# Optimization experiments

Hardware: AMD Instinct MI355X
Metric: run time of the kernel (lower is better)

## Reference

```python
import jax, jax.numpy as jnp
import numpy as np
from jax import lax

# init_kwargs constants
DO_TUBE = False
TAU = 0.3
ITERATIONS = 5
BLEND_FACTOR = 0.3


def _avg_pool3(x):
    """3x3x3 avg pool, stride 1, zero padding 1, count_include_pad=True.
    x: (n, h, w, d). Matches torch F.avg_pool3d(kernel=3, stride=1, padding=1)."""
    s = lax.reduce_window(x, 0.0, lax.add, (1, 3, 3, 3), (1, 1, 1, 1), 'SAME')
    return s * (1.0 / 27.0)


def setup_inputs() -> dict:
    key = jax.random.key(0)
    # binary mask (b, 1, h, w, d) as docstring requires
    u = jax.random.uniform(key, (2, 1, 256, 256, 256), dtype=jnp.float32)
    seg = (u > 0.5).astype(jnp.float32)
    return {"segmentation": seg}


def reference(segmentation):
    b, c, h, w, d = segmentation.shape
    x = segmentation.reshape(b * c, h, w, d)

    # NOTE: in the original code `mask` is never updated inside the iteration
    # loop, so every iteration adds the identical term; the loop over the
    # batch dim is also trivially batchable. Compute the per-iteration term
    # once (fully batched) and scale by ITERATIONS.
    eroded = -_avg_pool3(-x)            # differentiable erosion
    dilated = _avg_pool3(eroded)        # differentiable dilation
    diff = x - dilated
    term = jax.nn.sigmoid((diff - 0.5) / TAU) + diff  # soft_threshold + residual
    skeleton = ITERATIONS * term

    skeleton = skeleton.reshape(b, c, h, w, d)
    # DO_TUBE is False (the torch code path for True is broken for 5D input)
    skeleton = BLEND_FACTOR * segmentation + (1.0 - BLEND_FACTOR) * skeleton
    skeleton = jnp.round(jnp.clip(skeleton, 0.0, 1.0))
    return 1.0 - skeleton
```

## Files before the change

kernel.cpp:

```cpp
#include <hip/hip_runtime.h>
#include <stdint.h>


typedef float  vfloat4 __attribute__((ext_vector_type(4)));

#define CH 32
#define NCHUNK 8
#define BLOCKS 1024

__device__ __forceinline__ uint32_t row_pack(uint32_t b, const int ln) {
    uint32_t up = (uint32_t)__shfl_up((int)b, 1);
    uint32_t dn = (uint32_t)__shfl_down((int)b, 1);
    if (ln == 0)  up = 0u;
    if (ln == 63) dn = 0u;
    uint64_t W = (uint64_t)(up >> 16) | ((uint64_t)b << 16)
               | ((uint64_t)(dn & 0xffffu) << 48);
    uint64_t S = W + ((W >> 8) << 1) + (W >> 16) * 3u + ((W >> 24) << 1) + (W >> 32);
    uint32_t n = (uint32_t)S;
    if (ln == 0)  n -= (b & 0xffu);
    if (ln == 63) n -= (b & 0xff000000u);
    return n | (b << 7);
}

__device__ __forceinline__ uint32_t bits_of(const vfloat4 v) {
    return (v.x > 0.5f ? 0x1u : 0u) | (v.y > 0.5f ? 0x100u : 0u)
         | (v.z > 0.5f ? 0x10000u : 0u) | (v.w > 0.5f ? 0x1000000u : 0u);
}

__global__ __launch_bounds__(256) void skel_k1(const float* __restrict__ x,
                                               uint32_t* __restrict__ ws) {
    const int ln    = threadIdx.x & 63;
    const int wid   = (blockIdx.x << 2) | (threadIdx.x >> 6);
    const int chunk = wid & (NCHUNK - 1);
    const int slab  = wid >> 3;
    const int w0    = chunk * CH;
    const vfloat4* xs = (const vfloat4*)(x + (size_t)slab * 65536);
    uint32_t* os = ws + (size_t)slab * 16384;

    auto ldraw = [&](int wi) -> vfloat4 {
        int wc = wi < 0 ? 0 : (wi > 255 ? 255 : wi);
        return __builtin_nontemporal_load(&xs[wc * 64 + ln]);
    };
    auto packb = [&](vfloat4 v, int wi) -> uint32_t {
        uint32_t b = bits_of(v);
        return (wi >= 0 && wi < 256) ? b : 0u;
    };

    vfloat4 a0 = ldraw(w0 - 2), a1 = ldraw(w0 - 1), a2 = ldraw(w0),
            a3 = ldraw(w0 + 1), a4 = ldraw(w0 + 2);
    vfloat4 raw0 = ldraw(w0 + 3), raw1 = ldraw(w0 + 4),
            raw2 = ldraw(w0 + 5), raw3 = ldraw(w0 + 6);
    uint32_t r0 = row_pack(packb(a0, w0 - 2), ln);
    uint32_t r1 = row_pack(packb(a1, w0 - 1), ln);
    uint32_t r2 = row_pack(packb(a2, w0    ), ln);
    uint32_t r3 = row_pack(packb(a3, w0 + 1), ln);
    uint32_t r4 = row_pack(packb(a4, w0 + 2), ln);

    for (int g = 0; g < CH; g += 4) {
        vfloat4 n0 = ldraw(w0 + g + 7),  n1 = ldraw(w0 + g + 8),
                n2 = ldraw(w0 + g + 9),  n3 = ldraw(w0 + g + 10);
        vfloat4 cur[4] = {raw0, raw1, raw2, raw3};
        #pragma unroll
        for (int j = 0; j < 4; ++j) {
            const int w = w0 + g + j;
            uint32_t rn = row_pack(packb(cur[j], w + 3), ln);
            uint32_t m0 = r0 & 0x7f7f7f7fu, m1 = r1 & 0x7f7f7f7fu,
                     m2 = r2 & 0x7f7f7f7fu, m3 = r3 & 0x7f7f7f7fu,
                     m4 = r4 & 0x7f7f7f7fu;
            uint32_t s = m0 + (m1 << 1) + m2 * 3u + (m3 << 1) + m4;
            if (w == 0 || w == 255) s -= m2;
            s |= (r2 & 0x80808080u);
            os[w * 64 + ln] = s;
            r0 = r1; r1 = r2; r2 = r3; r3 = r4; r4 = rn;
        }
        raw0 = n0; raw1 = n1; raw2 = n2; raw3 = n3;
    }
}

__global__ __launch_bounds__(256) void skel_k2(const uint32_t* __restrict__ ws,
                                               vfloat4* __restrict__ out) {
    const int ln    = threadIdx.x & 63;
    const int wid   = (blockIdx.x << 2) | (threadIdx.x >> 6);
    const int chunk = wid & (NCHUNK - 1);
    const int col   = wid >> 3;
    const int wi    = col & 255, bi = col >> 8;
    const int h0    = chunk * CH;
    const uint32_t base = (uint32_t)bi * (1u << 22) + (uint32_t)wi * 64u + (uint32_t)ln;

    auto ld = [&](int hi) -> uint32_t {
        int hc = hi < 0 ? 0 : (hi > 255 ? 255 : hi);
        return ws[base + (uint32_t)hc * 16384u];
    };
    auto msk = [&](uint32_t q, int hi) -> uint32_t {
        return (hi >= 0 && hi < 256) ? q : 0u;
    };

    uint32_t q0 = msk(ld(h0 - 2), h0 - 2), q1 = msk(ld(h0 - 1), h0 - 1),
             q2 = ld(h0), q3 = ld(h0 + 1), q4 = ld(h0 + 2);
    uint32_t p0 = ld(h0 + 3), p1 = ld(h0 + 4), p2 = ld(h0 + 5), p3 = ld(h0 + 6);

    for (int g = 0; g < CH; g += 4) {
        uint32_t f0 = ld(h0 + g + 7),  f1 = ld(h0 + g + 8),
                 f2 = ld(h0 + g + 9),  f3 = ld(h0 + g + 10);
        uint32_t cur[4] = {p0, p1, p2, p3};
        #pragma unroll
        for (int j = 0; j < 4; ++j) {
            const int h = h0 + g + j;
            uint32_t qn = msk(cur[j], h + 3);
            uint32_t m0 = q0 & 0x7f7f7f7fu, m1 = q1 & 0x7f7f7f7fu,
                     m2 = q2 & 0x7f7f7f7fu, m3 = q3 & 0x7f7f7f7fu,
                     m4 = q4 & 0x7f7f7f7fu;
            uint32_t e0 = m0 & 0x00ff00ffu, e1 = m1 & 0x00ff00ffu,
                     e2 = m2 & 0x00ff00ffu, e3 = m3 & 0x00ff00ffu,
                     e4 = m4 & 0x00ff00ffu;
            uint32_t o0 = (m0 >> 8) & 0x00ff00ffu, o1 = (m1 >> 8) & 0x00ff00ffu,
                     o2 = (m2 >> 8) & 0x00ff00ffu, o3 = (m3 >> 8) & 0x00ff00ffu,
                     o4 = (m4 >> 8) & 0x00ff00ffu;
            uint32_t ae = e0 + (e1 << 1) + e2 * 3u + (e3 << 1) + e4;
            uint32_t ao = o0 + (o1 << 1) + o2 * 3u + (o3 << 1) + o4;
            if (h == 0 || h == 255) { ae -= e2; ao -= o2; }
            const uint32_t xb = q2;
            vfloat4 o;
            o.x = ((ae & 0xffffu) >= 9u && !((xb >> 7)  & 1u)) ? 1.0f : 0.0f;
            o.y = ((ao & 0xffffu) >= 9u && !((xb >> 15) & 1u)) ? 1.0f : 0.0f;
            o.z = ((ae >> 16)     >= 9u && !((xb >> 23) & 1u)) ? 1.0f : 0.0f;
            o.w = ((ao >> 16)     >= 9u && !((xb >> 31) & 1u)) ? 1.0f : 0.0f;
            __builtin_nontemporal_store(o, &out[base + (uint32_t)h * 16384u]);
            q0 = q1; q1 = q2; q2 = q3; q3 = q4; q4 = qn;
        }
        p0 = f0; p1 = f1; p2 = f2; p3 = f3;
    }
}

extern "C" void kernel_launch(void* const* d_in, const int* in_sizes, int n_in,
                              void* d_out, int out_size, void* d_ws, size_t ws_size,
                              hipStream_t stream) {
    const float* x = (const float*)d_in[0];
    uint32_t* ws = (uint32_t*)d_ws;
    skel_k1<<<BLOCKS, 256, 0, stream>>>(x, ws);
    skel_k2<<<BLOCKS, 256, 0, stream>>>(ws, (vfloat4*)d_out);
}
```

Measured before the change: 232.4 us.

## Fuse two-pass separable stencil into one kernel with h-row register tile

Replaces the two-kernel pipeline (w/d pass writing a packed workspace, then h pass) with one kernel. Each wave loads a 12-row h halo and slides along w, computing both stencil stages in registers. This removes the workspace round trip and a launch, but reads input rows redundantly (12 rows per 8 outputs) and greatly increases register pressure with fewer waves in flight.

```diff
diff --git a/kernel.cpp b/kernel.cpp
--- a/kernel.cpp
+++ b/kernel.cpp
@@ -2,11 +2,12 @@
 #include <stdint.h>
 
 
-typedef float  vfloat4 __attribute__((ext_vector_type(4)));
+typedef float vfloat4 __attribute__((ext_vector_type(4)));
 
-#define CH 32
-#define NCHUNK 8
-#define BLOCKS 1024
+#define CH 8
+#define HB 8
+#define NR 12
+#define BLOCKS 512
 
 __device__ __forceinline__ uint32_t row_pack(uint32_t b, const int ln) {
     uint32_t up = (uint32_t)__shfl_up((int)b, 1);
@@ -27,108 +28,104 @@
          | (v.z > 0.5f ? 0x10000u : 0u) | (v.w > 0.5f ? 0x1000000u : 0u);
 }
 
-__global__ __launch_bounds__(256) void skel_k1(const float* __restrict__ x,
-                                               uint32_t* __restrict__ ws) {
-    const int ln    = threadIdx.x & 63;
-    const int wid   = (blockIdx.x << 2) | (threadIdx.x >> 6);
-    const int chunk = wid & (NCHUNK - 1);
-    const int slab  = wid >> 3;
-    const int w0    = chunk * CH;
-    const vfloat4* xs = (const vfloat4*)(x + (size_t)slab * 65536);
-    uint32_t* os = ws + (size_t)slab * 16384;
+__global__ __launch_bounds__(256) void skel_fused(const float* __restrict__ x,
+                                                  vfloat4* __restrict__ out) {
+    const int ln  = threadIdx.x & 63;
+    const int wid = (blockIdx.x << 2) | (threadIdx.x >> 6);
+    const int wchunk =  wid        & 31;
+    const int hblk   = (wid >> 5)  & 31;
+    const int bi     =  wid >> 10;
+    const int w0 = wchunk * CH;
+    const int h0 = hblk * HB;
 
-    auto ldraw = [&](int wi) -> vfloat4 {
-        int wc = wi < 0 ? 0 : (wi > 255 ? 255 : wi);
-        return __builtin_nontemporal_load(&xs[wc * 64 + ln]);
+    const vfloat4* xb = (const vfloat4*)x + ((size_t)bi << 22);
+    vfloat4* ob = out + ((size_t)bi << 22);
+
+    uint32_t roff[NR];
+    uint32_t rok[NR];
+    #pragma unroll
+    for (int r = 0; r < NR; ++r) {
+        const int h  = h0 - 2 + r;
+        const int hc = h < 0 ? 0 : (h > 255 ? 255 : h);
+        roff[r] = (uint32_t)hc * 16384u;
+        rok[r]  = (h >= 0 && h <= 255) ? 0xffffffffu : 0u;
+    }
+
+    auto ld = [&](int r, int wi) -> vfloat4 {
+        const int wc = wi < 0 ? 0 : (wi > 255 ? 255 : wi);
+        return xb[roff[r] + (uint32_t)wc * 64u + (uint32_t)ln];
     };
-    auto packb = [&](vfloat4 v, int wi) -> uint32_t {
+    auto pk = [&](vfloat4 v, int r, int wi) -> uint32_t {
         uint32_t b = bits_of(v);
-        return (wi >= 0 && wi < 256) ? b : 0u;
+        b = (wi >= 0 && wi < 256) ? b : 0u;
+        return b & rok[r];
     };
 
-    vfloat4 a0 = ldraw(w0 - 2), a1 = ldraw(w0 - 1), a2 = ldraw(w0),
-            a3 = ldraw(w0 + 1), a4 = ldraw(w0 + 2);
-    vfloat4 raw0 = ldraw(w0 + 3), raw1 = ldraw(w0 + 4),
-            raw2 = ldraw(w0 + 5), raw3 = ldraw(w0 + 6);
-    uint32_t r0 = row_pack(packb(a0, w0 - 2), ln);
-    uint32_t r1 = row_pack(packb(a1, w0 - 1), ln);
-    uint32_t r2 = row_pack(packb(a2, w0    ), ln);
-    uint32_t r3 = row_pack(packb(a3, w0 + 1), ln);
-    uint32_t r4 = row_pack(packb(a4, w0 + 2), ln);
+    uint32_t win[NR][5];
+    #pragma unroll
+    for (int i = 0; i < 5; ++i) {
+        vfloat4 tmp[NR];
+        #pragma unroll
+        for (int r = 0; r < NR; ++r) tmp[r] = ld(r, w0 - 2 + i);
+        #pragma unroll
+        for (int r = 0; r < NR; ++r)
+            win[r][i] = row_pack(pk(tmp[r], r, w0 - 2 + i), ln);
+    }
+    vfloat4 nxt[NR];
+    #pragma unroll
+    for (int r = 0; r < NR; ++r) nxt[r] = ld(r, w0 + 3);
 
-    for (int g = 0; g < CH; g += 4) {
-        vfloat4 n0 = ldraw(w0 + g + 7),  n1 = ldraw(w0 + g + 8),
-                n2 = ldraw(w0 + g + 9),  n3 = ldraw(w0 + g + 10);
-        vfloat4 cur[4] = {raw0, raw1, raw2, raw3};
+    #pragma unroll 2
+    for (int j = 0; j < CH; ++j) {
+        const int w = w0 + j;
+
+        uint32_t t[NR];
         #pragma unroll
-        for (int j = 0; j < 4; ++j) {
-            const int w = w0 + g + j;
-            uint32_t rn = row_pack(packb(cur[j], w + 3), ln);
-            uint32_t m0 = r0 & 0x7f7f7f7fu, m1 = r1 & 0x7f7f7f7fu,
-                     m2 = r2 & 0x7f7f7f7fu, m3 = r3 & 0x7f7f7f7fu,
-                     m4 = r4 & 0x7f7f7f7fu;
+        for (int r = 0; r < NR; ++r) {
+            const uint32_t m0 = win[r][0] & 0x7f7f7f7fu, m1 = win[r][1] & 0x7f7f7f7fu,
+                           m2 = win[r][2] & 0x7f7f7f7fu, m3 = win[r][3] & 0x7f7f7f7fu,
+                           m4 = win[r][4] & 0x7f7f7f7fu;
             uint32_t s = m0 + (m1 << 1) + m2 * 3u + (m3 << 1) + m4;
             if (w == 0 || w == 255) s -= m2;
-            s |= (r2 & 0x80808080u);
-            os[w * 64 + ln] = s;
-            r0 = r1; r1 = r2; r2 = r3; r3 = r4; r4 = rn;
+            t[r] = s | (win[r][2] & 0x80808080u);
         }
-        raw0 = n0; raw1 = n1; raw2 = n2; raw3 = n3;
-    }
-}
 
-__global__ __launch_bounds__(256) void skel_k2(const uint32_t* __restrict__ ws,
-                                               vfloat4* __restrict__ out) {
-    const int ln    = threadIdx.x & 63;
-    const int wid   = (blockIdx.x << 2) | (threadIdx.x >> 6);
-    const int chunk = wid & (NCHUNK - 1);
-    const int col   = wid >> 3;
-    const int wi    = col & 255, bi = col >> 8;
-    const int h0    = chunk * CH;
-    const uint32_t base = (uint32_t)bi * (1u << 22) + (uint32_t)wi * 64u + (uint32_t)ln;
-
-    auto ld = [&](int hi) -> uint32_t {
-        int hc = hi < 0 ? 0 : (hi > 255 ? 255 : hi);
-        return ws[base + (uint32_t)hc * 16384u];
-    };
-    auto msk = [&](uint32_t q, int hi) -> uint32_t {
-        return (hi >= 0 && hi < 256) ? q : 0u;
-    };
-
-    uint32_t q0 = msk(ld(h0 - 2), h0 - 2), q1 = msk(ld(h0 - 1), h0 - 1),
-             q2 = ld(h0), q3 = ld(h0 + 1), q4 = ld(h0 + 2);
-    uint32_t p0 = ld(h0 + 3), p1 = ld(h0 + 4), p2 = ld(h0 + 5), p3 = ld(h0 + 6);
-
-    for (int g = 0; g < CH; g += 4) {
-        uint32_t f0 = ld(h0 + g + 7),  f1 = ld(h0 + g + 8),
-                 f2 = ld(h0 + g + 9),  f3 = ld(h0 + g + 10);
-        uint32_t cur[4] = {p0, p1, p2, p3};
         #pragma unroll
-        for (int j = 0; j < 4; ++j) {
-            const int h = h0 + g + j;
-            uint32_t qn = msk(cur[j], h + 3);
-            uint32_t m0 = q0 & 0x7f7f7f7fu, m1 = q1 & 0x7f7f7f7fu,
-                     m2 = q2 & 0x7f7f7f7fu, m3 = q3 & 0x7f7f7f7fu,
-                     m4 = q4 & 0x7f7f7f7fu;
-            uint32_t e0 = m0 & 0x00ff00ffu, e1 = m1 & 0x00ff00ffu,
-                     e2 = m2 & 0x00ff00ffu, e3 = m3 & 0x00ff00ffu,
-                     e4 = m4 & 0x00ff00ffu;
-            uint32_t o0 = (m0 >> 8) & 0x00ff00ffu, o1 = (m1 >> 8) & 0x00ff00ffu,
-                     o2 = (m2 >> 8) & 0x00ff00ffu, o3 = (m3 >> 8) & 0x00ff00ffu,
-                     o4 = (m4 >> 8) & 0x00ff00ffu;
+        for (int k = 0; k < HB; ++k) {
+            const int h = h0 + k;
+            const uint32_t m0 = t[k]   & 0x7f7f7f7fu, m1 = t[k+1] & 0x7f7f7f7fu,
+                           m2 = t[k+2] & 0x7f7f7f7fu, m3 = t[k+3] & 0x7f7f7f7fu,
+                           m4 = t[k+4] & 0x7f7f7f7fu;
+            const uint32_t e0 = m0 & 0x00ff00ffu, e1 = m1 & 0x00ff00ffu,
+                           e2 = m2 & 0x00ff00ffu, e3 = m3 & 0x00ff00ffu,
+                           e4 = m4 & 0x00ff00ffu;
+            const uint32_t o0 = (m0 >> 8) & 0x00ff00ffu, o1 = (m1 >> 8) & 0x00ff00ffu,
+                           o2 = (m2 >> 8) & 0x00ff00ffu, o3 = (m3 >> 8) & 0x00ff00ffu,
+                           o4 = (m4 >> 8) & 0x00ff00ffu;
             uint32_t ae = e0 + (e1 << 1) + e2 * 3u + (e3 << 1) + e4;
             uint32_t ao = o0 + (o1 << 1) + o2 * 3u + (o3 << 1) + o4;
             if (h == 0 || h == 255) { ae -= e2; ao -= o2; }
-            const uint32_t xb = q2;
+            const uint32_t xbit = t[k+2];
             vfloat4 o;
-            o.x = ((ae & 0xffffu) >= 9u && !((xb >> 7)  & 1u)) ? 1.0f : 0.0f;
-            o.y = ((ao & 0xffffu) >= 9u && !((xb >> 15) & 1u)) ? 1.0f : 0.0f;
-            o.z = ((ae >> 16)     >= 9u && !((xb >> 23) & 1u)) ? 1.0f : 0.0f;
-            o.w = ((ao >> 16)     >= 9u && !((xb >> 31) & 1u)) ? 1.0f : 0.0f;
-            __builtin_nontemporal_store(o, &out[base + (uint32_t)h * 16384u]);
-            q0 = q1; q1 = q2; q2 = q3; q3 = q4; q4 = qn;
+            o.x = ((ae & 0xffffu) >= 9u && !((xbit >> 7)  & 1u)) ? 1.0f : 0.0f;
+            o.y = ((ao & 0xffffu) >= 9u && !((xbit >> 15) & 1u)) ? 1.0f : 0.0f;
+            o.z = ((ae >> 16)     >= 9u && !((xbit >> 23) & 1u)) ? 1.0f : 0.0f;
+            o.w = ((ao >> 16)     >= 9u && !((xbit >> 31) & 1u)) ? 1.0f : 0.0f;
+            __builtin_nontemporal_store(
+                o, &ob[(uint32_t)h * 16384u + (uint32_t)w * 64u + (uint32_t)ln]);
         }
-        p0 = f0; p1 = f1; p2 = f2; p3 = f3;
+
+        #pragma unroll
+        for (int r = 0; r < NR; ++r) {
+            const uint32_t rn = row_pack(pk(nxt[r], r, w + 3), ln);
+            win[r][0] = win[r][1]; win[r][1] = win[r][2];
+            win[r][2] = win[r][3]; win[r][3] = win[r][4];
+            win[r][4] = rn;
+        }
+        if (j < CH - 1) {
+            #pragma unroll
+            for (int r = 0; r < NR; ++r) nxt[r] = ld(r, w + 4);
+        }
     }
 }
 
@@ -136,7 +133,6 @@
                               void* d_out, int out_size, void* d_ws, size_t ws_size,
                               hipStream_t stream) {
     const float* x = (const float*)d_in[0];
-    uint32_t* ws = (uint32_t*)d_ws;
-    skel_k1<<<BLOCKS, 256, 0, stream>>>(x, ws);
-    skel_k2<<<BLOCKS, 256, 0, stream>>>(ws, (vfloat4*)d_out);
+    (void)d_ws; (void)ws_size; (void)in_sizes; (void)n_in; (void)out_size;
+    skel_fused<<<BLOCKS, 256, 0, stream>>>(x, (vfloat4*)d_out);
 }
```

After: 254.6 us. 1.1x slower.
